# Performance work log

Measured on AMD Instinct MI355X. Metric: run time of the kernel, lower is better.

The kernel has to match this reference:

```python
import jax, jax.numpy as jnp
import numpy as np

D = 128        # num_hidden
NIN = 384      # num_in (edge feature dim)
FF = 4 * D     # dense inner dim
SCALE = 30.0
EPS = 1e-5     # haiku LayerNorm default

gelu = lambda x: jax.nn.gelu(x, approximate=False)

def _ln(x, g, o):
    mu = jnp.mean(x, axis=-1, keepdims=True)
    var = jnp.var(x, axis=-1, keepdims=True)
    return (x - mu) * jax.lax.rsqrt(var + EPS) * g + o

def setup_inputs() -> dict:
    key = jax.random.key(0)
    ks = jax.random.split(key, 12)
    B, N, K = 4, 2048, 48
    s = lambda fan_in: 1.0 / np.sqrt(fan_in)
    return {
        "h_V": jax.random.normal(ks[0], (B, N, D), jnp.float32),
        "h_E": jax.random.normal(ks[1], (B, N, K, NIN), jnp.float32),
        "mask_V": jnp.ones((B, N), jnp.float32),
        "mask_attend": jnp.ones((B, N, K), jnp.float32),
        "W1": jax.random.normal(ks[2], (D + NIN, D), jnp.float32) * s(D + NIN),
        "b1": jnp.zeros((D,), jnp.float32),
        "W2": jax.random.normal(ks[3], (D, D), jnp.float32) * s(D),
        "b2": jnp.zeros((D,), jnp.float32),
        "W3": jax.random.normal(ks[4], (D, D), jnp.float32) * s(D),
        "b3": jnp.zeros((D,), jnp.float32),
        "W_in": jax.random.normal(ks[5], (D, FF), jnp.float32) * s(D),
        "b_in": jnp.zeros((FF,), jnp.float32),
        "W_out": jax.random.normal(ks[6], (FF, D), jnp.float32) * s(FF),
        "b_out": jnp.zeros((D,), jnp.float32),
        "g1": jnp.ones((D,), jnp.float32),
        "o1": jnp.zeros((D,), jnp.float32),
        "g2": jnp.ones((D,), jnp.float32),
        "o2": jnp.zeros((D,), jnp.float32),
    }

def reference(h_V, h_E, mask_V, mask_attend, W1, b1, W2, b2, W3, b3,
              W_in, b_in, W_out, b_out, g1, o1, g2, o2):
    B, N, K, _ = h_E.shape
    # broadcast node feats over neighbors and concat with edge feats: (B,N,K,D+NIN)
    h_V_exp = jnp.broadcast_to(h_V[:, :, None, :], (B, N, K, h_V.shape[-1]))
    h_EV = jnp.concatenate([h_V_exp, h_E], axis=-1)
    h = gelu(h_EV @ W1 + b1)
    h = gelu(h @ W2 + b2)
    h_message = h @ W3 + b3                      # (B,N,K,D)
    h_message = mask_attend[..., None] * h_message
    dh = jnp.sum(h_message, axis=-2) / SCALE      # (B,N,D)
    h_V = _ln(h_V + dh, g1, o1)                   # dropout rate=0 -> identity
    dh = gelu(h_V @ W_in + b_in) @ W_out + b_out  # position-wise FFN
    h_V = _ln(h_V + dh, g2, o2)
    h_V = mask_V[..., None] * h_V
    return h_V
```

## Files before the change

kernel.cpp:

```cpp
#include <hip/hip_runtime.h>
#include <hip/hip_bf16.h>

typedef unsigned short u16;
typedef __attribute__((ext_vector_type(8))) short short8;
typedef __attribute__((ext_vector_type(4))) float f32x4;

#define SD   128
#define SNIN 384
#define SK   48
#define HPAD 136
#define FPAD 520

#define OFF_W1A   0
#define OFF_W1B   32768
#define OFF_W2    131072
#define OFF_W3    163840
#define OFF_WIN   196608
#define OFF_WOUT  327680

__device__ __forceinline__ u16 f2b(float f){
  union { float f; unsigned u; } v; v.f = f;
  unsigned r = (v.u + 0x7FFFu + ((v.u >> 16) & 1u)) >> 16;
  return (u16)r;
}
__device__ __forceinline__ short8 ldg8(const u16* p){
  return *reinterpret_cast<const short8*>(p);
}
__device__ __forceinline__ short8 pack8(float4 a, float4 b){
  union { unsigned u[4]; short8 s; } r;
  asm("v_cvt_pk_bf16_f32 %0, %1, %2" : "=v"(r.u[0]) : "v"(a.x), "v"(a.y));
  asm("v_cvt_pk_bf16_f32 %0, %1, %2" : "=v"(r.u[1]) : "v"(a.z), "v"(a.w));
  asm("v_cvt_pk_bf16_f32 %0, %1, %2" : "=v"(r.u[2]) : "v"(b.x), "v"(b.y));
  asm("v_cvt_pk_bf16_f32 %0, %1, %2" : "=v"(r.u[3]) : "v"(b.z), "v"(b.w));
  return r.s;
}
__device__ __forceinline__ short8 cvt8(const float* p){
  float4 a = *reinterpret_cast<const float4*>(p);
  float4 b = *reinterpret_cast<const float4*>(p + 4);
  return pack8(a, b);
}

__device__ __forceinline__ float gelu_f(float x){
  float xc = fminf(3.0f, fmaxf(-3.0f, x));
  float u  = xc*xc;
  float p  = fmaf(u, fmaf(u, fmaf(u, -4.81034e-4f, 1.185750e-2f), -1.1877797e-1f), 7.9165011e-1f);
  float t  = xc*p;
  float hx = 0.5f*x;
  return fmaf(t, hx, hx);
}

__global__ __launch_bounds__(256) void prep_pack(
    const float* __restrict__ W1, const float* __restrict__ W2, const float* __restrict__ W3,
    const float* __restrict__ Win, const float* __restrict__ Wout, u16* __restrict__ ws)
{
  int t = blockIdx.x*256 + threadIdx.x;
  const float* src; int stride, rowoff, NT; u16* dst; int local;
  if (t < 2048)       { src=W1;  stride=SD;  rowoff=0;   NT=8;  dst=ws+OFF_W1A/2;  local=t;       }
  else if (t < 8192)  { src=W1;  stride=SD;  rowoff=128; NT=8;  dst=ws+OFF_W1B/2;  local=t-2048;  }
  else if (t < 10240) { src=W2;  stride=SD;  rowoff=0;   NT=8;  dst=ws+OFF_W2/2;   local=t-8192;  }
  else if (t < 12288) { src=W3;  stride=SD;  rowoff=0;   NT=8;  dst=ws+OFF_W3/2;   local=t-10240; }
  else if (t < 20480) { src=Win; stride=512; rowoff=0;   NT=32; dst=ws+OFF_WIN/2;  local=t-12288; }
  else                { src=Wout;stride=SD;  rowoff=0;   NT=8;  dst=ws+OFF_WOUT/2; local=t-20480; }
  int lane = local & 63;
  int blk  = local >> 6;
  int nt = blk % NT, ks = blk / NT;
  int k0 = rowoff + ks*32 + (lane>>4)*8;
  int n  = nt*16 + (lane & 15);
  union { u16 a[8]; short8 v; } tmp;
  #pragma unroll
  for (int j=0;j<8;j++) tmp.a[j] = f2b(src[(size_t)(k0+j)*stride + n]);
  *reinterpret_cast<short8*>(dst + (size_t)local*8) = tmp.v;
}

__device__ __forceinline__ void mlp128(const u16* __restrict__ Bb, const u16* HHw,
                                       int l16, int quad, f32x4 acc[24])
{
  short8 bc[8], bn[8];
  #pragma unroll
  for (int nt=0;nt<8;nt++) bc[nt] = ldg8(Bb + ((size_t)nt*64)*8);
  #pragma unroll
  for (int ks=0; ks<4; ks++){
    if (ks < 3){
      #pragma unroll
      for (int nt=0;nt<8;nt++) bn[nt] = ldg8(Bb + ((size_t)((ks+1)*8+nt)*64)*8);
    }
    short8 af[3];
    #pragma unroll
    for (int mt=0; mt<3; mt++)
      af[mt] = *reinterpret_cast<const short8*>(&HHw[(size_t)(mt*16+l16)*HPAD + ks*32 + quad*8]);
    #pragma unroll
    for (int nt=0; nt<8; nt++)
      #pragma unroll
      for (int mt=0; mt<3; mt++)
        acc[mt*8+nt] = __builtin_amdgcn_mfma_f32_16x16x32_bf16(af[mt], bc[nt], acc[mt*8+nt], 0,0,0);
    if (ks < 3){
      #pragma unroll
      for (int nt=0;nt<8;nt++) bc[nt] = bn[nt];
    }
  }
}

#define LDA(BUF, kk) { _Pragma("unroll") for (int mt=0; mt<3; mt++){ \
    BUF[mt][0] = *reinterpret_cast<const float4*>(Ab + (size_t)mt*16*SNIN + (kk)*32); \
    BUF[mt][1] = *reinterpret_cast<const float4*>(Ab + (size_t)mt*16*SNIN + (kk)*32 + 4); } }

#define G1STEP(CUR, NXT, ks, PF) { \
    if (PF) LDA(NXT, (ks)+2); \
    short8 af[3]; \
    _Pragma("unroll") for (int mt=0; mt<3; mt++) af[mt] = pack8(CUR[mt][0], CUR[mt][1]); \
    _Pragma("unroll") for (int nt=0; nt<8; nt++){ \
      short8 bf = ldg8(Bb + ((size_t)((ks)*8+nt)*64)*8); \
      _Pragma("unroll") for (int mt=0; mt<3; mt++) \
        acc[mt*8+nt] = __builtin_amdgcn_mfma_f32_16x16x32_bf16(af[mt], bf, acc[mt*8+nt], 0,0,0); \
    } }

#define B1STEP(HB, ks) { \
    short8 af = pack8(HB[0], HB[1]); \
    _Pragma("unroll") for (int nt=0; nt<8; nt++){ \
      short8 bf = ldg8(Bb1 + ((size_t)((ks)*8+nt)*64)*8); \
      accb[nt] = __builtin_amdgcn_mfma_f32_16x16x32_bf16(af, bf, accb[nt], 0,0,0); \
    } }

__global__ __launch_bounds__(256, 2) void dec_nodes(
    const float* __restrict__ hV, const float* __restrict__ hE, const float* __restrict__ mAtt,
    const float* __restrict__ b1, const float* __restrict__ b2, const float* __restrict__ b3,
    const float* __restrict__ g1, const float* __restrict__ o1,
    const u16* __restrict__ ws, float* __restrict__ u_out)
{
  __shared__ u16 HH[4][SK*HPAD];

  const int tid  = threadIdx.x;
  const int w    = tid >> 6;
  const int lane = tid & 63;
  const int quad = lane >> 4;
  const int l16  = lane & 15;
  const int g    = blockIdx.x*4 + w;
  u16* HHw = HH[w];

  float base1v[8];
  {
    f32x4 accb[8];
    #pragma unroll
    for (int nt=0;nt<8;nt++) accb[nt] = (f32x4){0.f,0.f,0.f,0.f};
    const u16* Bb1 = ws + OFF_W1A/2 + (size_t)lane*8;
    const float* hp = hV + (size_t)g*SD + quad*8;
    float4 H0[2], H1[2], H2[2], H3[2];
    H0[0] = *reinterpret_cast<const float4*>(hp);       H0[1] = *reinterpret_cast<const float4*>(hp+4);
    H1[0] = *reinterpret_cast<const float4*>(hp+32);    H1[1] = *reinterpret_cast<const float4*>(hp+36);
    H2[0] = *reinterpret_cast<const float4*>(hp+64);    H2[1] = *reinterpret_cast<const float4*>(hp+68);
    H3[0] = *reinterpret_cast<const float4*>(hp+96);    H3[1] = *reinterpret_cast<const float4*>(hp+100);
    B1STEP(H0,0); B1STEP(H1,1); B1STEP(H2,2); B1STEP(H3,3);
    #pragma unroll
    for (int nt=0;nt<8;nt++) base1v[nt] = accb[nt][0] + b1[nt*16 + l16];
  }

  f32x4 acc[24];
  #pragma unroll
  for (int i=0;i<24;i++) acc[i] = (f32x4){0.f,0.f,0.f,0.f};
  {
    const float* Ab = hE + (size_t)g*(SK*SNIN) + (size_t)l16*SNIN + quad*8;
    const u16*  Bb = ws + OFF_W1B/2 + (size_t)lane*8;
    float4 A0[3][2], A1[3][2], A2[3][2];
    LDA(A0,0); LDA(A1,1);
    G1STEP(A0,A2,0,1);  G1STEP(A1,A0,1,1);  G1STEP(A2,A1,2,1);
    G1STEP(A0,A2,3,1);  G1STEP(A1,A0,4,1);  G1STEP(A2,A1,5,1);
    G1STEP(A0,A2,6,1);  G1STEP(A1,A0,7,1);  G1STEP(A2,A1,8,1);
    G1STEP(A0,A2,9,1);  G1STEP(A1,A0,10,0); G1STEP(A2,A1,11,0);
    #pragma unroll
    for (int mt=0; mt<3; mt++)
      #pragma unroll
      for (int nt=0; nt<8; nt++)
        #pragma unroll
        for (int i=0;i<4;i++){
          int row = mt*16 + quad*4 + i;
          HHw[row*HPAD + nt*16 + l16] = f2b(gelu_f(acc[mt*8+nt][i] + base1v[nt]));
        }
  }
  __syncthreads();

  #pragma unroll
  for (int i=0;i<24;i++) acc[i] = (f32x4){0.f,0.f,0.f,0.f};
  mlp128(ws + OFF_W2/2 + (size_t)lane*8, HHw, l16, quad, acc);
  __syncthreads();
  {
    #pragma unroll
    for (int mt=0; mt<3; mt++)
      #pragma unroll
      for (int nt=0; nt<8; nt++){
        float bb = b2[nt*16 + l16];
        #pragma unroll
        for (int i=0;i<4;i++){
          int row = mt*16 + quad*4 + i;
          HHw[row*HPAD + nt*16 + l16] = f2b(gelu_f(acc[mt*8+nt][i] + bb));
        }
      }
  }
  __syncthreads();

  #pragma unroll
  for (int i=0;i<24;i++) acc[i] = (f32x4){0.f,0.f,0.f,0.f};
  mlp128(ws + OFF_W3/2 + (size_t)lane*8, HHw, l16, quad, acc);
  float p[8];
  {
    #pragma unroll
    for (int nt=0;nt<8;nt++) p[nt] = 0.f;
    #pragma unroll
    for (int mt=0; mt<3; mt++)
      #pragma unroll
      for (int i=0;i<4;i++){
        float m = mAtt[(size_t)g*SK + mt*16 + quad*4 + i];
        #pragma unroll
        for (int nt=0; nt<8; nt++){
          float bb = b3[nt*16 + l16];
          p[nt] = fmaf(m, acc[mt*8+nt][i] + bb, p[nt]);
        }
      }
    #pragma unroll
    for (int nt=0;nt<8;nt++){
      p[nt] += __shfl_down(p[nt], 32, 64);
      p[nt] += __shfl_down(p[nt], 16, 64);
      p[nt]  = __shfl(p[nt], l16, 64);
    }
  }

  {
    float x[8];
    float s = 0.f, q = 0.f;
    #pragma unroll
    for (int nt=0;nt<8;nt++){
      x[nt] = hV[(size_t)g*SD + nt*16 + l16] + p[nt]*(1.0f/30.0f);
      s += x[nt]; q = fmaf(x[nt], x[nt], q);
    }
    #pragma unroll
    for (int off=1; off<64; off<<=1){ s += __shfl_xor(s, off, 64); q += __shfl_xor(q, off, 64); }
    float mu  = s * (1.0f/512.0f);
    float var = q * (1.0f/512.0f) - mu*mu;
    float rs  = rsqrtf(var + 1e-5f);
    #pragma unroll
    for (int k=0;k<2;k++){
      int nt = 2*quad + k;
      float uv = (x[nt]-mu)*rs*g1[nt*16+l16] + o1[nt*16+l16];
      u_out[(size_t)g*SD + nt*16 + l16] = uv;
    }
  }
}

__global__ __launch_bounds__(256) void ffn_ln(
    const float* __restrict__ b_in, const float* __restrict__ b_out,
    const float* __restrict__ g2, const float* __restrict__ o2, const float* __restrict__ mV,
    const u16* __restrict__ ws, float* __restrict__ uo)
{
  __shared__ u16 fS[16*FPAD];
  __shared__ float dS[16][132];
  const int tid = threadIdx.x, w = tid>>6, lane = tid&63, quad = lane>>4, l16 = lane&15;
  const int m0 = blockIdx.x*16;

  short8 afr[4];
  const float* Ap = uo + (size_t)(m0 + l16)*SD + quad*8;
  #pragma unroll
  for (int ks=0; ks<4; ks++) afr[ks] = cvt8(Ap + ks*32);

  {
    f32x4 acc[8];
    #pragma unroll
    for (int t=0;t<8;t++) acc[t] = (f32x4){0.f,0.f,0.f,0.f};
    const u16* Bp = ws + OFF_WIN/2 + ((size_t)(w*8)*64 + lane)*8;
    #pragma unroll
    for (int ks=0; ks<4; ks++){
      #pragma unroll
      for (int t=0;t<8;t++){
        short8 bf = ldg8(Bp + ((size_t)ks*32 + t)*512);
        acc[t] = __builtin_amdgcn_mfma_f32_16x16x32_bf16(afr[ks], bf, acc[t], 0,0,0);
      }
    }
    #pragma unroll
    for (int t=0;t<8;t++){
      int coln = w*128 + t*16 + l16;
      float bi = b_in[coln];
      #pragma unroll
      for (int i=0;i<4;i++)
        fS[(quad*4+i)*FPAD + coln] = f2b(gelu_f(acc[t][i] + bi));
    }
  }
  __syncthreads();

  {
    f32x4 acc2[2];
    acc2[0] = (f32x4){0.f,0.f,0.f,0.f};
    acc2[1] = (f32x4){0.f,0.f,0.f,0.f};
    const u16* Bo = ws + OFF_WOUT/2 + (size_t)lane*8;
    #pragma unroll
    for (int ks=0; ks<16; ks++){
      const short8 af = *reinterpret_cast<const short8*>(&fS[l16*FPAD + ks*32 + quad*8]);
      #pragma unroll
      for (int j=0;j<2;j++){
        short8 bf = ldg8(Bo + ((size_t)ks*8 + (w*2+j))*512);
        acc2[j] = __builtin_amdgcn_mfma_f32_16x16x32_bf16(af, bf, acc2[j], 0,0,0);
      }
    }
    #pragma unroll
    for (int j=0;j<2;j++){
      int cl = (w*2+j)*16 + l16;
      float bo = b_out[cl];
      #pragma unroll
      for (int i=0;i<4;i++)
        dS[quad*4+i][cl] = acc2[j][i] + bo;
    }
  }
  __syncthreads();

  {
    int rl = w*4 + quad;
    int r  = m0 + rl;
    float xv[8]; float s = 0.f, q = 0.f;
    #pragma unroll
    for (int t=0;t<8;t++){
      xv[t] = uo[(size_t)r*SD + t*16 + l16] + dS[rl][t*16 + l16];
      s += xv[t]; q = fmaf(xv[t], xv[t], q);
    }
    #pragma unroll
    for (int mk=1; mk<16; mk<<=1){ s += __shfl_xor(s, mk, 64); q += __shfl_xor(q, mk, 64); }
    float mu  = s * (1.0f/128.0f);
    float var = q * (1.0f/128.0f) - mu*mu;
    float rs  = rsqrtf(var + 1e-5f);
    float mv  = mV[r];
    #pragma unroll
    for (int t=0;t<8;t++){
      int cl = t*16 + l16;
      uo[(size_t)r*SD + cl] = mv * ((xv[t]-mu)*rs*g2[cl] + o2[cl]);
    }
  }
}

extern "C" void kernel_launch(void* const* d_in, const int* in_sizes, int n_in,
                              void* d_out, int out_size, void* d_ws, size_t ws_size,
                              hipStream_t stream) {
  (void)n_in; (void)out_size; (void)ws_size;
  const float* hV    = (const float*)d_in[0];
  const float* hE    = (const float*)d_in[1];
  const float* mV    = (const float*)d_in[2];
  const float* mAtt  = (const float*)d_in[3];
  const float* W1    = (const float*)d_in[4];
  const float* b1    = (const float*)d_in[5];
  const float* W2    = (const float*)d_in[6];
  const float* b2    = (const float*)d_in[7];
  const float* W3    = (const float*)d_in[8];
  const float* b3    = (const float*)d_in[9];
  const float* Win   = (const float*)d_in[10];
  const float* b_in  = (const float*)d_in[11];
  const float* Wout  = (const float*)d_in[12];
  const float* b_out = (const float*)d_in[13];
  const float* g1    = (const float*)d_in[14];
  const float* o1    = (const float*)d_in[15];
  const float* g2    = (const float*)d_in[16];
  const float* o2    = (const float*)d_in[17];
  u16*   ws   = (u16*)d_ws;
  float* outp = (float*)d_out;
  const int NG = in_sizes[0] / SD;

  hipLaunchKernelGGL(prep_pack, dim3(112), dim3(256), 0, stream, W1, W2, W3, Win, Wout, ws);
  hipLaunchKernelGGL(dec_nodes, dim3(NG/4), dim3(256), 0, stream,
                     hV, hE, mAtt, b1, b2, b3, g1, o1, ws, outp);
  hipLaunchKernelGGL(ffn_ln, dim3(NG/16), dim3(256), 0, stream,
                     b_in, b_out, g2, o2, mV, ws, outp);
}
```

Measured before the change: 904.5 us.

## Split each node across four waves with LDS-staged edge loads

The edge-MLP kernel previously gave each wave one whole node. It now gives each 256-thread block one node, and each wave computes two of the eight 16-column output tiles. Edge features are streamed into double-buffered LDS through global_load_lds with an XOR swizzle, and the hidden activations are shared in a swizzled LDS tile. The LayerNorm reduction is combined across waves through shared memory. This cuts per-wave register pressure (occupancy hint raised from 2 to 4) and overlaps the hE stream with compute, at the cost of many more block-level barriers and four times as many blocks.

Result: faster. 862.5 us (-4.6%).

```diff
diff --git a/kernel.cpp b/kernel.cpp
--- a/kernel.cpp
+++ b/kernel.cpp
@@ -8,7 +8,6 @@
 #define SD   128
 #define SNIN 384
 #define SK   48
-#define HPAD 136
 #define FPAD 520
 
 #define OFF_W1A   0
@@ -38,6 +37,10 @@
   float4 a = *reinterpret_cast<const float4*>(p);
   float4 b = *reinterpret_cast<const float4*>(p + 4);
   return pack8(a, b);
+}
+__device__ __forceinline__ void gl_lds16(const float* g, float* l){
+  __builtin_amdgcn_global_load_lds((const __attribute__((address_space(1))) void*)g,
+                                   (__attribute__((address_space(3))) void*)l, 16, 0, 0);
 }
 
 __device__ __forceinline__ float gelu_f(float x){
@@ -72,177 +75,195 @@
   *reinterpret_cast<short8*>(dst + (size_t)local*8) = tmp.v;
 }
 
-__device__ __forceinline__ void mlp128(const u16* __restrict__ Bb, const u16* HHw,
-                                       int l16, int quad, f32x4 acc[24])
-{
-  short8 bc[8], bn[8];
-  #pragma unroll
-  for (int nt=0;nt<8;nt++) bc[nt] = ldg8(Bb + ((size_t)nt*64)*8);
-  #pragma unroll
-  for (int ks=0; ks<4; ks++){
-    if (ks < 3){
-      #pragma unroll
-      for (int nt=0;nt<8;nt++) bn[nt] = ldg8(Bb + ((size_t)((ks+1)*8+nt)*64)*8);
-    }
-    short8 af[3];
-    #pragma unroll
-    for (int mt=0; mt<3; mt++)
-      af[mt] = *reinterpret_cast<const short8*>(&HHw[(size_t)(mt*16+l16)*HPAD + ks*32 + quad*8]);
-    #pragma unroll
-    for (int nt=0; nt<8; nt++)
-      #pragma unroll
-      for (int mt=0; mt<3; mt++)
-        acc[mt*8+nt] = __builtin_amdgcn_mfma_f32_16x16x32_bf16(af[mt], bc[nt], acc[mt*8+nt], 0,0,0);
-    if (ks < 3){
-      #pragma unroll
-      for (int nt=0;nt<8;nt++) bc[nt] = bn[nt];
-    }
-  }
-}
-
-#define LDA(BUF, kk) { _Pragma("unroll") for (int mt=0; mt<3; mt++){ \
-    BUF[mt][0] = *reinterpret_cast<const float4*>(Ab + (size_t)mt*16*SNIN + (kk)*32); \
-    BUF[mt][1] = *reinterpret_cast<const float4*>(Ab + (size_t)mt*16*SNIN + (kk)*32 + 4); } }
-
-#define G1STEP(CUR, NXT, ks, PF) { \
-    if (PF) LDA(NXT, (ks)+2); \
-    short8 af[3]; \
-    _Pragma("unroll") for (int mt=0; mt<3; mt++) af[mt] = pack8(CUR[mt][0], CUR[mt][1]); \
-    _Pragma("unroll") for (int nt=0; nt<8; nt++){ \
-      short8 bf = ldg8(Bb + ((size_t)((ks)*8+nt)*64)*8); \
-      _Pragma("unroll") for (int mt=0; mt<3; mt++) \
-        acc[mt*8+nt] = __builtin_amdgcn_mfma_f32_16x16x32_bf16(af[mt], bf, acc[mt*8+nt], 0,0,0); \
-    } }
-
-#define B1STEP(HB, ks) { \
-    short8 af = pack8(HB[0], HB[1]); \
-    _Pragma("unroll") for (int nt=0; nt<8; nt++){ \
-      short8 bf = ldg8(Bb1 + ((size_t)((ks)*8+nt)*64)*8); \
-      accb[nt] = __builtin_amdgcn_mfma_f32_16x16x32_bf16(af, bf, accb[nt], 0,0,0); \
-    } }
-
-__global__ __launch_bounds__(256, 2) void dec_nodes(
+__global__ __launch_bounds__(256, 4) void dec_nodes(
     const float* __restrict__ hV, const float* __restrict__ hE, const float* __restrict__ mAtt,
     const float* __restrict__ b1, const float* __restrict__ b2, const float* __restrict__ b3,
     const float* __restrict__ g1, const float* __restrict__ o1,
     const u16* __restrict__ ws, float* __restrict__ u_out)
 {
-  __shared__ u16 HH[4][SK*HPAD];
+  __shared__ __align__(16) float STG[2][1536];
+  __shared__ __align__(16) u16   HHs[48*128];
+  __shared__ float LNS[8];
 
   const int tid  = threadIdx.x;
   const int w    = tid >> 6;
   const int lane = tid & 63;
   const int quad = lane >> 4;
   const int l16  = lane & 15;
-  const int g    = blockIdx.x*4 + w;
-  u16* HHw = HH[w];
-
-  float base1v[8];
-  {
-    f32x4 accb[8];
-    #pragma unroll
-    for (int nt=0;nt<8;nt++) accb[nt] = (f32x4){0.f,0.f,0.f,0.f};
+  const int g    = blockIdx.x;
+  const int n0   = w*2;
+
+  const float* gsrcl = hE + (size_t)g*(SK*SNIN) + (size_t)(lane>>3)*SNIN
+                          + (size_t)(((lane&7) ^ (lane>>3))*4);
+
+  #define STAGE(ks, buf) { \
+    if (w < 2){ gl_lds16(gsrcl + (size_t)(2*w)*8*SNIN   + (ks)*32, &STG[buf][(2*w)*256]);   \
+                gl_lds16(gsrcl + (size_t)(2*w+1)*8*SNIN + (ks)*32, &STG[buf][(2*w+1)*256]); } \
+    else      { gl_lds16(gsrcl + (size_t)(w+2)*8*SNIN   + (ks)*32, &STG[buf][(w+2)*256]);   } }
+
+  STAGE(0, 0);
+
+  float base1v[2];
+  {
+    f32x4 accb[2] = {(f32x4){0.f,0.f,0.f,0.f},(f32x4){0.f,0.f,0.f,0.f}};
+    const float* hp = hV + (size_t)g*SD + quad*8;
     const u16* Bb1 = ws + OFF_W1A/2 + (size_t)lane*8;
-    const float* hp = hV + (size_t)g*SD + quad*8;
-    float4 H0[2], H1[2], H2[2], H3[2];
-    H0[0] = *reinterpret_cast<const float4*>(hp);       H0[1] = *reinterpret_cast<const float4*>(hp+4);
-    H1[0] = *reinterpret_cast<const float4*>(hp+32);    H1[1] = *reinterpret_cast<const float4*>(hp+36);
-    H2[0] = *reinterpret_cast<const float4*>(hp+64);    H2[1] = *reinterpret_cast<const float4*>(hp+68);
-    H3[0] = *reinterpret_cast<const float4*>(hp+96);    H3[1] = *reinterpret_cast<const float4*>(hp+100);
-    B1STEP(H0,0); B1STEP(H1,1); B1STEP(H2,2); B1STEP(H3,3);
-    #pragma unroll
-    for (int nt=0;nt<8;nt++) base1v[nt] = accb[nt][0] + b1[nt*16 + l16];
-  }
-
-  f32x4 acc[24];
-  #pragma unroll
-  for (int i=0;i<24;i++) acc[i] = (f32x4){0.f,0.f,0.f,0.f};
-  {
-    const float* Ab = hE + (size_t)g*(SK*SNIN) + (size_t)l16*SNIN + quad*8;
-    const u16*  Bb = ws + OFF_W1B/2 + (size_t)lane*8;
-    float4 A0[3][2], A1[3][2], A2[3][2];
-    LDA(A0,0); LDA(A1,1);
-    G1STEP(A0,A2,0,1);  G1STEP(A1,A0,1,1);  G1STEP(A2,A1,2,1);
-    G1STEP(A0,A2,3,1);  G1STEP(A1,A0,4,1);  G1STEP(A2,A1,5,1);
-    G1STEP(A0,A2,6,1);  G1STEP(A1,A0,7,1);  G1STEP(A2,A1,8,1);
-    G1STEP(A0,A2,9,1);  G1STEP(A1,A0,10,0); G1STEP(A2,A1,11,0);
-    #pragma unroll
-    for (int mt=0; mt<3; mt++)
-      #pragma unroll
-      for (int nt=0; nt<8; nt++)
+    #pragma unroll
+    for (int ks=0; ks<4; ks++){
+      short8 af = cvt8(hp + ks*32);
+      #pragma unroll
+      for (int j=0;j<2;j++){
+        short8 bf = ldg8(Bb1 + ((size_t)(ks*8 + n0 + j)*64)*8);
+        accb[j] = __builtin_amdgcn_mfma_f32_16x16x32_bf16(af, bf, accb[j], 0,0,0);
+      }
+    }
+    #pragma unroll
+    for (int j=0;j<2;j++) base1v[j] = accb[j][0] + b1[(n0+j)*16 + l16];
+  }
+
+  const u16* BbG1 = ws + OFF_W1B/2 + (size_t)lane*8;
+  short8 bq0 = ldg8(BbG1 + ((size_t)(n0)*64)*8);
+  short8 bq1 = ldg8(BbG1 + ((size_t)(n0+1)*64)*8);
+  __syncthreads();
+
+  f32x4 acc[3][2];
+  #pragma unroll
+  for (int mt=0;mt<3;mt++){ acc[mt][0]=(f32x4){0.f,0.f,0.f,0.f}; acc[mt][1]=(f32x4){0.f,0.f,0.f,0.f}; }
+
+  #pragma unroll
+  for (int ks=0; ks<12; ks++){
+    short8 bn0, bn1;
+    if (ks < 11){
+      bn0 = ldg8(BbG1 + ((size_t)((ks+1)*8 + n0)*64)*8);
+      bn1 = ldg8(BbG1 + ((size_t)((ks+1)*8 + n0+1)*64)*8);
+      STAGE(ks+1, (ks+1)&1);
+    }
+    const float* bufF = STG[ks&1];
+    short8 af[3];
+    #pragma unroll
+    for (int mt=0;mt<3;mt++){
+      int row = mt*16 + l16;
+      int sp0 = (2*quad) ^ (l16 & 7);
+      float4 a = *reinterpret_cast<const float4*>(bufF + row*32 + sp0*4);
+      float4 b = *reinterpret_cast<const float4*>(bufF + row*32 + (sp0^1)*4);
+      af[mt] = pack8(a, b);
+    }
+    #pragma unroll
+    for (int mt=0;mt<3;mt++){
+      acc[mt][0] = __builtin_amdgcn_mfma_f32_16x16x32_bf16(af[mt], bq0, acc[mt][0], 0,0,0);
+      acc[mt][1] = __builtin_amdgcn_mfma_f32_16x16x32_bf16(af[mt], bq1, acc[mt][1], 0,0,0);
+    }
+    __syncthreads();
+    if (ks < 11){ bq0 = bn0; bq1 = bn1; }
+  }
+
+  #pragma unroll
+  for (int mt=0; mt<3; mt++)
+    #pragma unroll
+    for (int j=0; j<2; j++)
+      #pragma unroll
+      for (int i=0;i<4;i++){
+        int row = mt*16 + quad*4 + i;
+        int col = (n0+j)*16 + l16;
+        HHs[row*128 + (((col>>3) ^ (row&15))<<3) + (col&7)] = f2b(gelu_f(acc[mt][j][i] + base1v[j]));
+      }
+  __syncthreads();
+
+  #pragma unroll
+  for (int mt=0;mt<3;mt++){ acc[mt][0]=(f32x4){0.f,0.f,0.f,0.f}; acc[mt][1]=(f32x4){0.f,0.f,0.f,0.f}; }
+  {
+    const u16* Bb = ws + OFF_W2/2 + (size_t)lane*8;
+    #pragma unroll
+    for (int ks=0; ks<4; ks++){
+      short8 afm[3];
+      #pragma unroll
+      for (int mt=0; mt<3; mt++){
+        int row = mt*16 + l16;
+        int sp  = (ks*4 + quad) ^ l16;
+        afm[mt] = *reinterpret_cast<const short8*>(HHs + row*128 + sp*8);
+      }
+      #pragma unroll
+      for (int j=0;j<2;j++){
+        short8 bf = ldg8(Bb + ((size_t)(ks*8 + n0 + j)*64)*8);
         #pragma unroll
-        for (int i=0;i<4;i++){
-          int row = mt*16 + quad*4 + i;
-          HHw[row*HPAD + nt*16 + l16] = f2b(gelu_f(acc[mt*8+nt][i] + base1v[nt]));
-        }
-  }
-  __syncthreads();
-
-  #pragma unroll
-  for (int i=0;i<24;i++) acc[i] = (f32x4){0.f,0.f,0.f,0.f};
-  mlp128(ws + OFF_W2/2 + (size_t)lane*8, HHw, l16, quad, acc);
-  __syncthreads();
-  {
-    #pragma unroll
-    for (int mt=0; mt<3; mt++)
-      #pragma unroll
-      for (int nt=0; nt<8; nt++){
-        float bb = b2[nt*16 + l16];
+        for (int mt=0;mt<3;mt++)
+          acc[mt][j] = __builtin_amdgcn_mfma_f32_16x16x32_bf16(afm[mt], bf, acc[mt][j], 0,0,0);
+      }
+    }
+  }
+  __syncthreads();
+  #pragma unroll
+  for (int mt=0; mt<3; mt++)
+    #pragma unroll
+    for (int j=0; j<2; j++){
+      float bb = b2[(n0+j)*16 + l16];
+      #pragma unroll
+      for (int i=0;i<4;i++){
+        int row = mt*16 + quad*4 + i;
+        int col = (n0+j)*16 + l16;
+        HHs[row*128 + (((col>>3) ^ (row&15))<<3) + (col&7)] = f2b(gelu_f(acc[mt][j][i] + bb));
+      }
+    }
+  __syncthreads();
+
+  #pragma unroll
+  for (int mt=0;mt<3;mt++){ acc[mt][0]=(f32x4){0.f,0.f,0.f,0.f}; acc[mt][1]=(f32x4){0.f,0.f,0.f,0.f}; }
+  {
+    const u16* Bb = ws + OFF_W3/2 + (size_t)lane*8;
+    #pragma unroll
+    for (int ks=0; ks<4; ks++){
+      short8 afm[3];
+      #pragma unroll
+      for (int mt=0; mt<3; mt++){
+        int row = mt*16 + l16;
+        int sp  = (ks*4 + quad) ^ l16;
+        afm[mt] = *reinterpret_cast<const short8*>(HHs + row*128 + sp*8);
+      }
+      #pragma unroll
+      for (int j=0;j<2;j++){
+        short8 bf = ldg8(Bb + ((size_t)(ks*8 + n0 + j)*64)*8);
         #pragma unroll
-        for (int i=0;i<4;i++){
-          int row = mt*16 + quad*4 + i;
-          HHw[row*HPAD + nt*16 + l16] = f2b(gelu_f(acc[mt*8+nt][i] + bb));
-        }
-      }
-  }
-  __syncthreads();
-
-  #pragma unroll
-  for (int i=0;i<24;i++) acc[i] = (f32x4){0.f,0.f,0.f,0.f};
-  mlp128(ws + OFF_W3/2 + (size_t)lane*8, HHw, l16, quad, acc);
-  float p[8];
-  {
-    #pragma unroll
-    for (int nt=0;nt<8;nt++) p[nt] = 0.f;
+        for (int mt=0;mt<3;mt++)
+          acc[mt][j] = __builtin_amdgcn_mfma_f32_16x16x32_bf16(afm[mt], bf, acc[mt][j], 0,0,0);
+      }
+    }
+  }
+  float p0 = 0.f, p1 = 0.f;
+  {
+    float b3v0 = b3[(n0)*16 + l16], b3v1 = b3[(n0+1)*16 + l16];
     #pragma unroll
     for (int mt=0; mt<3; mt++)
       #pragma unroll
       for (int i=0;i<4;i++){
         float m = mAtt[(size_t)g*SK + mt*16 + quad*4 + i];
-        #pragma unroll
-        for (int nt=0; nt<8; nt++){
-          float bb = b3[nt*16 + l16];
-          p[nt] = fmaf(m, acc[mt*8+nt][i] + bb, p[nt]);
-        }
-      }
-    #pragma unroll
-    for (int nt=0;nt<8;nt++){
-      p[nt] += __shfl_down(p[nt], 32, 64);
-      p[nt] += __shfl_down(p[nt], 16, 64);
-      p[nt]  = __shfl(p[nt], l16, 64);
-    }
-  }
-
-  {
-    float x[8];
-    float s = 0.f, q = 0.f;
-    #pragma unroll
-    for (int nt=0;nt<8;nt++){
-      x[nt] = hV[(size_t)g*SD + nt*16 + l16] + p[nt]*(1.0f/30.0f);
-      s += x[nt]; q = fmaf(x[nt], x[nt], q);
-    }
+        p0 = fmaf(m, acc[mt][0][i] + b3v0, p0);
+        p1 = fmaf(m, acc[mt][1][i] + b3v1, p1);
+      }
+    p0 += __shfl_down(p0, 32, 64); p0 += __shfl_down(p0, 16, 64); p0 = __shfl(p0, l16, 64);
+    p1 += __shfl_down(p1, 32, 64); p1 += __shfl_down(p1, 16, 64); p1 = __shfl(p1, l16, 64);
+  }
+
+  {
+    float x0 = hV[(size_t)g*SD + (n0)*16   + l16] + p0*(1.0f/30.0f);
+    float x1 = hV[(size_t)g*SD + (n0+1)*16 + l16] + p1*(1.0f/30.0f);
+    float s = x0 + x1;
+    float q = fmaf(x0, x0, x1*x1);
     #pragma unroll
     for (int off=1; off<64; off<<=1){ s += __shfl_xor(s, off, 64); q += __shfl_xor(q, off, 64); }
+    if (lane == 0){ LNS[w] = s; LNS[4+w] = q; }
+    __syncthreads();
+    s = LNS[0]+LNS[1]+LNS[2]+LNS[3];
+    q = LNS[4]+LNS[5]+LNS[6]+LNS[7];
     float mu  = s * (1.0f/512.0f);
     float var = q * (1.0f/512.0f) - mu*mu;
     float rs  = rsqrtf(var + 1e-5f);
-    #pragma unroll
-    for (int k=0;k<2;k++){
-      int nt = 2*quad + k;
-      float uv = (x[nt]-mu)*rs*g1[nt*16+l16] + o1[nt*16+l16];
-      u_out[(size_t)g*SD + nt*16 + l16] = uv;
-    }
-  }
+    if (quad == 0){
+      int c0 = (n0)*16 + l16, c1 = (n0+1)*16 + l16;
+      u_out[(size_t)g*SD + c0] = (x0-mu)*rs*g1[c0] + o1[c0];
+      u_out[(size_t)g*SD + c1] = (x1-mu)*rs*g1[c1] + o1[c1];
+    }
+  }
+  #undef STAGE
 }
 
 __global__ __launch_bounds__(256) void ffn_ln(
@@ -359,7 +380,7 @@
   const int NG = in_sizes[0] / SD;
 
   hipLaunchKernelGGL(prep_pack, dim3(112), dim3(256), 0, stream, W1, W2, W3, Win, Wout, ws);
-  hipLaunchKernelGGL(dec_nodes, dim3(NG/4), dim3(256), 0, stream,
+  hipLaunchKernelGGL(dec_nodes, dim3(NG), dim3(256), 0, stream,
                      hV, hE, mAtt, b1, b2, b3, g1, o1, ws, outp);
   hipLaunchKernelGGL(ffn_ln, dim3(NG/16), dim3(256), 0, stream,
                      b_in, b_out, g2, o2, mV, ws, outp);
```
